# Optimization experiments

Measured on AMD Instinct MI355X. Metric: run time of the kernel, lower is better.

The kernel has to match this reference:

```python
import jax, jax.numpy as jnp
import numpy as np

EPS = 1e-12
LN_EPS = 1e-5
RIDGE = 0.01
M, L, T = 256, 4096, 2048


def setup_inputs() -> dict:
    key = jax.random.key(0)
    ks = jax.random.split(key, 16)
    inp = {
        "gamma": jax.random.uniform(ks[0], (L,), dtype=jnp.float32),
        "A_re": jax.random.normal(ks[1], (M, L), dtype=jnp.float32),
        "A_im": jax.random.normal(ks[2], (M, L), dtype=jnp.float32),
        "X_re": jax.random.normal(ks[3], (M, T), dtype=jnp.float32),
        "X_im": jax.random.normal(ks[4], (M, T), dtype=jnp.float32),
        # LayerNorm(L) params
        "ln_w": jnp.ones((L,), jnp.float32),
        "ln_b": jnp.zeros((L,), jnp.float32),
        # MultiheadAttention(embed_dim=1, num_heads=1): in_proj [3,1]->[3], out_proj [1,1]->[1]
        "in_w": jax.random.normal(ks[5], (3,), dtype=jnp.float32),
        "in_b": jnp.zeros((3,), jnp.float32),
        "out_w": jax.random.normal(ks[6], (1,), dtype=jnp.float32),
        "out_b": jnp.zeros((1,), jnp.float32),
        # gate Linear(L, L)
        "gate_W": jax.random.normal(ks[7], (L, L), dtype=jnp.float32) * (1.0 / np.sqrt(L)),
        "gate_b": jnp.zeros((L,), jnp.float32),
        # learned scalars
        "delta": jnp.float32(0.5),
        "lmbda": jnp.float32(0.01),
    }
    return inp


def _iaa_forward(gamma, A_re, A_im, X_re, X_im, ln_w, ln_b, in_w, in_b,
                 out_w, out_b, gate_W, gate_b, delta, lmbda):
    A = (A_re + 1j * A_im).astype(jnp.complex64)      # [M, L]
    X = (X_re + 1j * X_im).astype(jnp.complex64)      # [M, T]
    p = gamma                                         # [L]

    # R = A diag(p) A^H + ridge * I   (MxM)
    AP = A * p[None, :].astype(A.dtype)
    R = AP @ A.conj().T + RIDGE * jnp.eye(M, dtype=A.dtype)
    Rinv = jnp.linalg.inv(R)                          # [M, M]

    Ah = A.conj().T                                   # [L, M]
    ARi = Ah @ Rinv                                   # [L, M]
    S = ARi @ X                                       # [L, T]
    q = jnp.sum(jnp.abs(S) ** 2, axis=1)              # [L]
    d = jnp.real(jnp.sum(ARi * Ah, axis=1))           # [L]
    v = q / (d + EPS)

    # constrain_gamma -> sigmoid(delta); use_residual
    dlt = jax.nn.sigmoid(delta)
    u = p + dlt * (v - p)

    # LayerNorm over the full length-L vector
    mu = jnp.mean(u)
    var = jnp.mean((u - mu) ** 2)
    u_p = (u - mu) / jnp.sqrt(var + LN_EPS) * ln_w + ln_b

    # MultiheadAttention(embed_dim=1, num_heads=1) over seq of L tokens, scale = 1/sqrt(1) = 1
    qv = u_p * in_w[0] + in_b[0]                      # [L]
    kv = u_p * in_w[1] + in_b[1]
    vv = u_p * in_w[2] + in_b[2]
    scores = qv[:, None] * kv[None, :]                # [L, L]
    attn = jax.nn.softmax(scores, axis=-1)
    attn_out = (attn @ vv) * out_w[0] + out_b[0]      # [L]

    # gating on u (pre-layernorm), as in the torch code
    g = jax.nn.sigmoid(gate_W @ u + gate_b)           # Linear: u @ W.T + b, u is 1-D -> W @ u + b
    r = g * v + (1.0 - g) * p

    s = r + attn_out
    return jax.nn.relu(s - lmbda)


def reference(gamma, A_re, A_im, X_re, X_im, ln_w, ln_b, in_w, in_b,
              out_w, out_b, gate_W, gate_b, delta, lmbda):
    return _iaa_forward(gamma, A_re, A_im, X_re, X_im, ln_w, ln_b, in_w, in_b,
                        out_w, out_b, gate_W, gate_b, delta, lmbda)
```

## Files before the change

### kernel.cpp

```cpp
#include <hip/hip_runtime.h>
#include <hip/hip_bf16.h>
#include <math.h>

#define MM 256
#define LL 4096
#define TT 2048

typedef __attribute__((ext_vector_type(8))) short bf16x8;
typedef __attribute__((ext_vector_type(4))) float f32x4;
typedef __attribute__((ext_vector_type(4))) unsigned short us4;
typedef unsigned short ushort_t;

#define OFF_Q      262144
#define OFF_D      266240
#define OFF_V      270336
#define OFF_U      274432
#define OFF_UP     278528
#define OFF_RINVP  290816
#define OFF_GP     421888
#define OFF_APL    552960
#define OFF_XPL    2650112
#define OFF_ATP    3698688
#define OFF_WTP    5795840
#define OFF_PA     5795840
#define OFF_PX     8417280
#define OFF_E0P    9990144
#define OFF_EAP    10252288
#define OFF_EBP    10514432
#define OFF_XAT    10776576
#define OFF_XBT    10907648

#define MFMA3(ACC, AH, AL, BH, BL)                                              \
  ACC = __builtin_amdgcn_mfma_f32_16x16x32_bf16(AH, BH, ACC, 0, 0, 0);          \
  ACC = __builtin_amdgcn_mfma_f32_16x16x32_bf16(AH, BL, ACC, 0, 0, 0);          \
  ACC = __builtin_amdgcn_mfma_f32_16x16x32_bf16(AL, BH, ACC, 0, 0, 0);

__device__ __forceinline__ void split_bf16(float x, ushort_t& h, ushort_t& l) {
  __hip_bfloat16 bh = __float2bfloat16(x);
  h = *(ushort_t*)&bh;
  __hip_bfloat16 bl = __float2bfloat16(x - __bfloat162float(bh));
  l = *(ushort_t*)&bl;
}
__device__ __forceinline__ float bfu2f(ushort_t u) {
  unsigned v = ((unsigned)u) << 16;
  float f;
  __builtin_memcpy(&f, &v, 4);
  return f;
}

__device__ __forceinline__ void tile_ij(int t, int& ti, int& tj) {
  float f = sqrtf(8.0f * (float)t + 1.0f);
  ti = (int)((f - 1.0f) * 0.5f + 0.001f);
  tj = t - ((ti * (ti + 1)) >> 1);
}

__device__ __forceinline__ float wave_red_sum(float v) {
#pragma unroll
  for (int o = 32; o > 0; o >>= 1) v += __shfl_down(v, o);
  return v;
}
__device__ __forceinline__ float wave_red_max(float v) {
#pragma unroll
  for (int o = 32; o > 0; o >>= 1) v = fmaxf(v, __shfl_down(v, o));
  return v;
}
__device__ float blk_red_sum(float v) {
  __shared__ float sh[4];
  int lane = threadIdx.x & 63, wv = threadIdx.x >> 6;
  v = wave_red_sum(v);
  __syncthreads();
  if (lane == 0) sh[wv] = v;
  __syncthreads();
  return sh[0] + sh[1] + sh[2] + sh[3];
}
__device__ float blk_red_max(float v) {
  __shared__ float shm[4];
  int lane = threadIdx.x & 63, wv = threadIdx.x >> 6;
  v = wave_red_max(v);
  __syncthreads();
  if (lane == 0) shm[wv] = v;
  __syncthreads();
  return fmaxf(fmaxf(shm[0], shm[1]), fmaxf(shm[2], shm[3]));
}

__device__ __forceinline__ float2 r_mirror(const float2* __restrict__ R, int i, int j) {
  if ((i >> 6) >= (j >> 6)) return R[i * 256 + j];
  float2 r = R[j * 256 + i];
  r.y = -r.y;
  return r;
}

__global__ __launch_bounds__(256) void k_prep(float* __restrict__ ws,
                                              const float* __restrict__ Are,
                                              const float* __restrict__ Aim,
                                              const float* __restrict__ Xre,
                                              const float* __restrict__ Xim,
                                              const float* __restrict__ gamma) {
  __shared__ float tr[32][33], ti[32][33];
  int bid = blockIdx.x, tid = threadIdx.x;
  if (bid < 8) {
    ((float4*)(ws + OFF_Q))[bid * 256 + tid] = make_float4(0.f, 0.f, 0.f, 0.f);
  } else if (bid < 1032) {
    int i4 = (bid - 8) * 256 + tid;
    ushort_t* dst = (ushort_t*)(ws + OFF_APL);
    float4 re = ((const float4*)Are)[i4];
    float4 im = ((const float4*)Aim)[i4];
    float4 ga = ((const float4*)gamma)[i4 & (LL / 4 - 1)];
    float sr[4] = {re.x * sqrtf(ga.x), re.y * sqrtf(ga.y), re.z * sqrtf(ga.z), re.w * sqrtf(ga.w)};
    float si[4] = {im.x * sqrtf(ga.x), im.y * sqrtf(ga.y), im.z * sqrtf(ga.z), im.w * sqrtf(ga.w)};
    us4 hr, lr, hi, li;
#pragma unroll
    for (int e = 0; e < 4; ++e) {
      ushort_t h, l;
      split_bf16(sr[e], h, l); hr[e] = h; lr[e] = l;
      split_bf16(si[e], h, l); hi[e] = h; li[e] = l;
    }
    size_t o = (size_t)i4 * 4;
    *(us4*)(dst + o) = hr;
    *(us4*)(dst + (size_t)MM * LL + o) = lr;
    *(us4*)(dst + 2 * (size_t)MM * LL + o) = hi;
    *(us4*)(dst + 3 * (size_t)MM * LL + o) = li;
  } else if (bid < 1544) {
    int i4 = (bid - 1032) * 256 + tid;
    ushort_t* dst = (ushort_t*)(ws + OFF_XPL);
    float4 re = ((const float4*)Xre)[i4];
    float4 im = ((const float4*)Xim)[i4];
    float fr[4] = {re.x, re.y, re.z, re.w};
    float fi[4] = {im.x, im.y, im.z, im.w};
    us4 hr, lr, hi, li;
#pragma unroll
    for (int e = 0; e < 4; ++e) {
      ushort_t h, l;
      split_bf16(fr[e], h, l); hr[e] = h; lr[e] = l;
      split_bf16(fi[e], h, l); hi[e] = h; li[e] = l;
    }
    size_t o = (size_t)i4 * 4;
    *(us4*)(dst + o) = hr;
    *(us4*)(dst + (size_t)MM * TT + o) = lr;
    *(us4*)(dst + 2 * (size_t)MM * TT + o) = hi;
    *(us4*)(dst + 3 * (size_t)MM * TT + o) = li;
  } else {
    int b2 = bid - 1544;
    ushort_t* dst = (ushort_t*)(ws + OFF_ATP);
    int c0 = (b2 & 127) * 32, r0 = (b2 >> 7) * 32;
    int tx = tid & 31, tg = tid >> 5;
#pragma unroll
    for (int i = 0; i < 4; ++i) {
      int r = tg + 8 * i;
      tr[r][tx] = Are[(size_t)(r0 + r) * LL + c0 + tx];
      ti[r][tx] = Aim[(size_t)(r0 + r) * LL + c0 + tx];
    }
    __syncthreads();
#pragma unroll
    for (int i = 0; i < 4; ++i) {
      int rr = tg + 8 * i;
      size_t o = (size_t)(c0 + rr) * 256 + r0 + tx;
      ushort_t h, l;
      split_bf16(tr[tx][rr], h, l);
      dst[o] = h;
      dst[o + 1048576] = l;
      split_bf16(ti[tx][rr], h, l);
      dst[o + 2097152] = h;
      dst[o + 3145728] = l;
    }
  }
}

__global__ __launch_bounds__(256, 4) void k_gram_both(float* __restrict__ ws) {
  __shared__ __align__(16) ushort_t sA[4][64][40];
  __shared__ __align__(16) ushort_t sB[4][64][40];
  const int ti_lu[10] = {0, 1, 1, 2, 2, 2, 3, 3, 3, 3};
  const int tj_lu[10] = {0, 0, 1, 0, 1, 2, 0, 1, 2, 3};
  int bid = blockIdx.x;
  const ushort_t* pl;
  float2* P;
  int K, tile, ksplit;
  size_t PS;
  if (bid < 320) {
    pl = (const ushort_t*)(ws + OFF_APL);
    P = (float2*)(ws + OFF_PA) + (size_t)bid * 4096;
    K = LL;
    PS = (size_t)MM * LL;
    tile = bid % 10;
    ksplit = bid / 10;
  } else {
    int b2 = bid - 320;
    pl = (const ushort_t*)(ws + OFF_XPL);
    P = (float2*)(ws + OFF_PX) + (size_t)b2 * 4096;
    K = TT;
    PS = (size_t)MM * TT;
    tile = b2 % 10;
    ksplit = b2 / 10;
  }
  int kbeg = ksplit * 128;
  int i0 = ti_lu[tile] * 64, j0 = tj_lu[tile] * 64;
  bool diag = (i0 == j0);
  int tid = threadIdx.x;
  int lane = tid & 63, wv = tid >> 6;
  int srow = tid >> 2, sslot = tid & 3;
  int arow = wv * 16 + (lane & 15);
  int kq = (lane >> 4) * 8;
  f32x4 z = {0.f, 0.f, 0.f, 0.f};
  f32x4 Zrr[4], Zri[4], Zir[4], Zii[4];
#pragma unroll
  for (int s = 0; s < 4; ++s) { Zrr[s] = z; Zri[s] = z; Zir[s] = z; Zii[s] = z; }

  for (int chunk = 0; chunk < 4; ++chunk) {
    int k0 = kbeg + chunk * 32;
    __syncthreads();
#pragma unroll
    for (int p = 0; p < 4; ++p) {
      *(bf16x8*)&sA[p][srow][sslot * 8] =
          *(const bf16x8*)(pl + p * PS + (size_t)(i0 + srow) * K + k0 + sslot * 8);
      if (!diag)
        *(bf16x8*)&sB[p][srow][sslot * 8] =
            *(const bf16x8*)(pl + p * PS + (size_t)(j0 + srow) * K + k0 + sslot * 8);
    }
    __syncthreads();
    bf16x8 arh = *(const bf16x8*)&sA[0][arow][kq];
    bf16x8 arl = *(const bf16x8*)&sA[1][arow][kq];
    bf16x8 aih = *(const bf16x8*)&sA[2][arow][kq];
    bf16x8 ail = *(const bf16x8*)&sA[3][arow][kq];
    ushort_t(*bs)[64][40] = diag ? sA : sB;
#pragma unroll
    for (int s = 0; s < 4; ++s) {
      int brow = s * 16 + (lane & 15);
      bf16x8 brh = *(const bf16x8*)&bs[0][brow][kq];
      bf16x8 brl = *(const bf16x8*)&bs[1][brow][kq];
      bf16x8 bih = *(const bf16x8*)&bs[2][brow][kq];
      bf16x8 bil = *(const bf16x8*)&bs[3][brow][kq];
      MFMA3(Zrr[s], arh, arl, brh, brl);
      MFMA3(Zri[s], arh, arl, bih, bil);
      MFMA3(Zir[s], aih, ail, brh, brl);
      MFMA3(Zii[s], aih, ail, bih, bil);
    }
  }
  int lrb = wv * 16 + (lane >> 4) * 4;
#pragma unroll
  for (int s = 0; s < 4; ++s) {
    int lc = s * 16 + (lane & 15);
#pragma unroll
    for (int r = 0; r < 4; ++r) {
      float re = Zrr[s][r] + Zii[s][r];
      float im = Zir[s][r] - Zri[s][r];
      P[(lrb + r) * 64 + lc] = make_float2(re, im);
    }
  }
}

__global__ __launch_bounds__(256) void k_reduce(float* __restrict__ ws) {
  int bid = blockIdx.x, tid = threadIdx.x;
  if (bid < 160) {
    const float2* PA = (const float2*)(ws + OFF_PA);
    float2* R2 = (float2*)ws;
    int t = bid >> 4;
    int e = ((bid & 15) << 8) + tid;
    float sx = 0.f, sy = 0.f;
#pragma unroll 4
    for (int k = 0; k < 32; ++k) {
      float2 p = PA[(size_t)(k * 10 + t) * 4096 + e];
      sx += p.x; sy += p.y;
    }
    int ti, tj;
    tile_ij(t, ti, tj);
    int i = ti * 64 + (e >> 6), j = tj * 64 + (e & 63);
    if (i == j) sx += 0.01f;
    R2[i * 256 + j] = make_float2(sx, sy);
  } else {
    const float2* PX = (const float2*)(ws + OFF_PX);
    ushort_t* dst = (ushort_t*)(ws + OFF_GP);
    int idx = (bid - 160) * 256 + tid;
    int i = idx >> 8, j = idx & 255;
    int ii = i, jj = j;
    float sgn = 1.f;
    if ((i >> 6) < (j >> 6)) { ii = j; jj = i; sgn = -1.f; }
    int ti = ii >> 6, tj = jj >> 6;
    int t = ((ti * (ti + 1)) >> 1) + tj;
    int e = ((ii & 63) << 6) + (jj & 63);
    float sx = 0.f, sy = 0.f;
#pragma unroll 4
    for (int k = 0; k < 16; ++k) {
      float2 p = PX[(size_t)(k * 10 + t) * 4096 + e];
      sx += p.x; sy += p.y;
    }
    sy *= sgn;
    ushort_t h, l;
    split_bf16(sx, h, l);
    dst[idx] = h;
    dst[idx + 65536] = l;
    split_bf16(sy, h, l);
    dst[idx + 131072] = h;
    dst[idx + 196608] = l;
  }
}

__global__ __launch_bounds__(256) void k_n1p(float* __restrict__ ws) {
  const float2* R = (const float2*)ws;
  ushort_t* e0 = (ushort_t*)(ws + OFF_E0P);
  ushort_t* e0t = e0 + 262144;
  ushort_t* x1t = (ushort_t*)(ws + OFF_XAT);
  int idx = blockIdx.x * 256 + threadIdx.x;
  int i = idx >> 8, j = idx & 255;
  float Dii = R[i * 257].x, Djj = R[j * 257].x;
  float2 r = r_mirror(R, i, j);
  float dl = (i == j) ? 1.0f : 0.0f;
  float ex = dl - r.x / Dii, ey = -r.y / Dii;
  float xx = (dl + ex) / Djj, xy = ey / Djj;
  int rm = i * 256 + j, trn = j * 256 + i;
  ushort_t h, l;
  split_bf16(ex, h, l);
  e0[rm] = h; e0[rm + 65536] = l;
  e0t[trn] = h; e0t[trn + 65536] = l;
  split_bf16(ey, h, l);
  e0[rm + 131072] = h; e0[rm + 196608] = l;
  e0t[trn + 131072] = h; e0t[trn + 196608] = l;
  split_bf16(xx, h, l);
  x1t[trn] = h; x1t[trn + 65536] = l;
  split_bf16(xy, h, l);
  x1t[trn + 131072] = h; x1t[trn + 196608] = l;
}

__global__ __launch_bounds__(256) void k_prim(const ushort_t* __restrict__ Arm,
                                              const ushort_t* __restrict__ BtrE,
                                              const ushort_t* __restrict__ BtrX,
                                              const ushort_t* __restrict__ AddX,
                                              ushort_t* __restrict__ EoutRm,
                                              ushort_t* __restrict__ EoutTr,
                                              ushort_t* __restrict__ XoutTr,
                                              ushort_t* __restrict__ XoutRm,
                                              int nEjobs) {
  __shared__ __align__(16) ushort_t sB[4][32][40];
  int job = blockIdx.x;
  bool isE = job < nEjobs;
  int b = isE ? job : job - nEjobs;
  const ushort_t* Bp = isE ? BtrE : BtrX;
  const ushort_t* Add = isE ? (const ushort_t*)nullptr : AddX;
  ushort_t* Otr = isE ? EoutTr : XoutTr;
  ushort_t* Orm = isE ? EoutRm : XoutRm;
  int j0 = (b & 7) * 32, i0 = (b >> 3) * 64;
  int tid = threadIdx.x;
  int lane = tid & 63, wv = tid >> 6;
  int spos = tid & 127;
  int srow = spos >> 2, sslot = spos & 3;
  int p0 = (tid >> 7) * 2;
  int m = i0 + wv * 16 + (lane & 15);
  int kq = (lane >> 4) * 8;
  f32x4 z = {0.f, 0.f, 0.f, 0.f};
  f32x4 Zrr[2], Zri[2], Zir[2], Zii[2];
#pragma unroll
  for (int s = 0; s < 2; ++s) { Zrr[s] = z; Zri[s] = z; Zir[s] = z; Zii[s] = z; }
  for (int k0 = 0; k0 < 256; k0 += 32) {
    __syncthreads();
    {
      size_t bo = (size_t)(j0 + srow) * 256 + k0 + sslot * 8;
      *(bf16x8*)&sB[p0][srow][sslot * 8] =
          *(const bf16x8*)(Bp + (size_t)p0 * 65536 + bo);
      *(bf16x8*)&sB[p0 + 1][srow][sslot * 8] =
          *(const bf16x8*)(Bp + (size_t)(p0 + 1) * 65536 + bo);
    }
    __syncthreads();
    size_t ao = (size_t)m * 256 + k0 + kq;
    bf16x8 arh = *(const bf16x8*)(Arm + ao);
    bf16x8 arl = *(const bf16x8*)(Arm + 65536 + ao);
    bf16x8 aih = *(const bf16x8*)(Arm + 131072 + ao);
    bf16x8 ail = *(const bf16x8*)(Arm + 196608 + ao);
#pragma unroll
    for (int s = 0; s < 2; ++s) {
      int brow = s * 16 + (lane & 15);
      bf16x8 brh = *(const bf16x8*)&sB[0][brow][kq];
      bf16x8 brl = *(const bf16x8*)&sB[1][brow][kq];
      bf16x8 bih = *(const bf16x8*)&sB[2][brow][kq];
      bf16x8 bil = *(const bf16x8*)&sB[3][brow][kq];
      MFMA3(Zrr[s], arh, arl, brh, brl);
      MFMA3(Zri[s], arh, arl, bih, bil);
      MFMA3(Zir[s], aih, ail, brh, brl);
      MFMA3(Zii[s], aih, ail, bih, bil);
    }
  }
  int rbase = i0 + wv * 16 + (lane >> 4) * 4;
#pragma unroll
  for (int s = 0; s < 2; ++s) {
    int col = j0 + s * 16 + (lane & 15);
    size_t wo = (size_t)col * 256 + rbase;
    us4 adr, adl, adi, adj;
    if (Add) {
      adr = *(const us4*)(Add + wo);
      adl = *(const us4*)(Add + 65536 + wo);
      adi = *(const us4*)(Add + 131072 + wo);
      adj = *(const us4*)(Add + 196608 + wo);
    }
    us4 hr, lr, hi, li;
#pragma unroll
    for (int r = 0; r < 4; ++r) {
      float re = Zrr[s][r] - Zii[s][r];
      float im = Zri[s][r] + Zir[s][r];
      if (Add) {
        re += bfu2f(adr[r]) + bfu2f(adl[r]);
        im += bfu2f(adi[r]) + bfu2f(adj[r]);
      }
      ushort_t h, l;
      split_bf16(re, h, l); hr[r] = h; lr[r] = l;
      split_bf16(im, h, l); hi[r] = h; li[r] = l;
    }
    if (Otr) {
      *(us4*)(Otr + wo) = hr;
      *(us4*)(Otr + 65536 + wo) = lr;
      *(us4*)(Otr + 131072 + wo) = hi;
      *(us4*)(Otr + 196608 + wo) = li;
    }
    if (Orm) {
#pragma unroll
      for (int r = 0; r < 4; ++r) {
        size_t o = (size_t)(rbase + r) * 256 + col;
        Orm[o] = hr[r];
        Orm[o + 65536] = lr[r];
        Orm[o + 131072] = hi[r];
        Orm[o + 196608] = li[r];
      }
    }
  }
}

__global__ __launch_bounds__(256) void k_wide_mfma(const ushort_t* __restrict__ Ap,
                                                   const ushort_t* __restrict__ Bp,
                                                   const float* __restrict__ AuxRe,
                                                   const float* __restrict__ AuxIm,
                                                   ushort_t* __restrict__ WTout,
                                                   float* __restrict__ dq, int mode) {
  __shared__ __align__(16) ushort_t sB[4][32][40];
  const ushort_t* arh_p = Ap;
  const ushort_t* arl_p = Ap + 65536;
  const ushort_t* aih_p = Ap + 131072;
  const ushort_t* ail_p = Ap + 196608;
  const ushort_t* brh_p = Bp;
  const ushort_t* brl_p = Bp + 1048576;
  const ushort_t* bih_p = Bp + 2097152;
  const ushort_t* bil_p = Bp + 3145728;
  int job = blockIdx.x;
  int j0 = (job & 127) * 32;
  int i0 = (job >> 7) * 64;
  int tid = threadIdx.x;
  int lane = tid & 63, wv = tid >> 6;
  int spos = tid & 127;
  int srow = spos >> 2, sslot = spos & 3;
  int p0 = (tid >> 7) * 2;
  const ushort_t* bp0 = (p0 == 0) ? brh_p : bih_p;
  const ushort_t* bp1 = (p0 == 0) ? brl_p : bil_p;
  int m = i0 + wv * 16 + (lane & 15);
  int kq = (lane >> 4) * 8;
  f32x4 z = {0.f, 0.f, 0.f, 0.f};
  f32x4 Zrr[2], Zri[2], Zir[2], Zii[2];
#pragma unroll
  for (int s = 0; s < 2; ++s) { Zrr[s] = z; Zri[s] = z; Zir[s] = z; Zii[s] = z; }
  for (int k0 = 0; k0 < 256; k0 += 32) {
    __syncthreads();
    {
      size_t bo = (size_t)(j0 + srow) * 256 + k0 + sslot * 8;
      *(bf16x8*)&sB[p0][srow][sslot * 8] = *(const bf16x8*)(bp0 + bo);
      *(bf16x8*)&sB[p0 + 1][srow][sslot * 8] = *(const bf16x8*)(bp1 + bo);
    }
    __syncthreads();
    size_t ao = (size_t)m * 256 + k0 + kq;
    bf16x8 arh = *(const bf16x8*)(arh_p + ao);
    bf16x8 arl = *(const bf16x8*)(arl_p + ao);
    bf16x8 aih = *(const bf16x8*)(aih_p + ao);
    bf16x8 ail = *(const bf16x8*)(ail_p + ao);
#pragma unroll
    for (int s = 0; s < 2; ++s) {
      int brow = s * 16 + (lane & 15);
      bf16x8 brh = *(const bf16x8*)&sB[0][brow][kq];
      bf16x8 brl = *(const bf16x8*)&sB[1][brow][kq];
      bf16x8 bih = *(const bf16x8*)&sB[2][brow][kq];
      bf16x8 bil = *(const bf16x8*)&sB[3][brow][kq];
      MFMA3(Zrr[s], arh, arl, brh, brl);
      MFMA3(Zri[s], arh, arl, bih, bil);
      MFMA3(Zir[s], aih, ail, brh, brl);
      MFMA3(Zii[s], aih, ail, bih, bil);
    }
  }
  int rbase = i0 + wv * 16 + (lane >> 4) * 4;
#pragma unroll
  for (int s = 0; s < 2; ++s) {
    int col = j0 + s * 16 + (lane & 15);
    size_t wo = (size_t)col * 256 + rbase;
    float part = 0.f;
    if (mode == 0) {
      us4 hr, lr, hi, li;
#pragma unroll
      for (int r = 0; r < 4; ++r) {
        float re = Zrr[s][r] - Zii[s][r];
        float im = Zri[s][r] + Zir[s][r];
        ushort_t h, l;
        split_bf16(re, h, l);
        hr[r] = h; lr[r] = l;
        split_bf16(im, h, l);
        hi[r] = h; li[r] = l;
        size_t o = (size_t)(rbase + r) * LL + col;
        part += re * AuxRe[o] - im * AuxIm[o];
      }
      *(us4*)(WTout + wo) = hr;
      *(us4*)(WTout + 1048576 + wo) = lr;
      *(us4*)(WTout + 2097152 + wo) = hi;
      *(us4*)(WTout + 3145728 + wo) = li;
    } else {
      us4 wh = *(const us4*)(brh_p + wo);
      us4 wl = *(const us4*)(brl_p + wo);
      us4 wih = *(const us4*)(bih_p + wo);
      us4 wil = *(const us4*)(bil_p + wo);
#pragma unroll
      for (int r = 0; r < 4; ++r) {
        float re = Zrr[s][r] - Zii[s][r];
        float im = Zri[s][r] + Zir[s][r];
        float wx = bfu2f(wh[r]) + bfu2f(wl[r]);
        float wy = bfu2f(wih[r]) + bfu2f(wil[r]);
        part += wx * re + wy * im;
      }
    }
    part += __shfl_down(part, 32);
    part += __shfl_down(part, 16);
    if ((lane >> 4) == 0) atomicAdd(dq + col, part);
  }
}

__global__ __launch_bounds__(1024) void k_uvln(float* __restrict__ ws,
                                               const float* __restrict__ gamma,
                                               const float* __restrict__ delta,
                                               const float* __restrict__ lnw,
                                               const float* __restrict__ lnb) {
  __shared__ float sh[16];
  int tid = threadIdx.x, lane = tid & 63, wv = tid >> 6;
  float4 q4 = ((const float4*)(ws + OFF_Q))[tid];
  float4 d4 = ((const float4*)(ws + OFF_D))[tid];
  float4 g4 = ((const float4*)gamma)[tid];
  float dlt = 1.0f / (1.0f + expf(-delta[0]));
  float v0 = q4.x / (d4.x + 1e-12f), v1 = q4.y / (d4.y + 1e-12f);
  float v2 = q4.z / (d4.z + 1e-12f), v3 = q4.w / (d4.w + 1e-12f);
  float u0 = g4.x + dlt * (v0 - g4.x), u1 = g4.y + dlt * (v1 - g4.y);
  float u2 = g4.z + dlt * (v2 - g4.z), u3 = g4.w + dlt * (v3 - g4.w);
  ((float4*)(ws + OFF_V))[tid] = make_float4(v0, v1, v2, v3);
  ((float4*)(ws + OFF_U))[tid] = make_float4(u0, u1, u2, u3);
  float s = wave_red_sum(u0 + u1 + u2 + u3);
  if (lane == 0) sh[wv] = s;
  __syncthreads();
  float mu = 0.f;
#pragma unroll
  for (int w = 0; w < 16; ++w) mu += sh[w];
  mu *= (1.0f / LL);
  __syncthreads();
  float d0 = u0 - mu, d1 = u1 - mu, d2 = u2 - mu, d3 = u3 - mu;
  float s2 = wave_red_sum(d0 * d0 + d1 * d1 + d2 * d2 + d3 * d3);
  if (lane == 0) sh[wv] = s2;
  __syncthreads();
  float var = 0.f;
#pragma unroll
  for (int w = 0; w < 16; ++w) var += sh[w];
  var *= (1.0f / LL);
  float inv = rsqrtf(var + 1e-5f);
  float4 w4 = ((const float4*)lnw)[tid];
  float4 b4 = ((const float4*)lnb)[tid];
  ((float4*)(ws + OFF_UP))[tid] =
      make_float4(d0 * inv * w4.x + b4.x, d1 * inv * w4.y + b4.y,
                  d2 * inv * w4.z + b4.z, d3 * inv * w4.w + b4.w);
}

__global__ __launch_bounds__(256) void k_gateattn(const float* __restrict__ ws,
                                                  const float* __restrict__ Wg,
                                                  const float* __restrict__ gb,
                                                  const float* __restrict__ inw,
                                                  const float* __restrict__ inb,
                                                  const float* __restrict__ outw,
                                                  const float* __restrict__ outb,
                                                  const float* __restrict__ gamma,
                                                  const float* __restrict__ lmbda,
                                                  float* __restrict__ out) {
  const float* uvec = ws + OFF_U;
  const float* up = ws + OFF_UP;
  const float* vvec = ws + OFF_V;
  int i = blockIdx.x, tid = threadIdx.x;
  const float4* wr = (const float4*)(Wg + (size_t)i * LL);
  const float4* u4 = (const float4*)uvec;
  float s = 0.f;
  for (int j = tid; j < LL / 4; j += 256) {
    float4 w = wr[j], x = u4[j];
    s += w.x * x.x + w.y * x.y + w.z * x.z + w.w * x.w;
  }
  float tot = blk_red_sum(s);
  float g = 1.0f / (1.0f + expf(-(tot + gb[i])));
  float qv = up[i] * inw[0] + inb[0];
  float w1 = inw[1], b1 = inb[1], w2 = inw[2], b2 = inb[2];
  const float4* up4 = (const float4*)up;
  float mx = -3.4e38f;
  for (int j = tid; j < LL / 4; j += 256) {
    float4 u = up4[j];
    mx = fmaxf(mx, fmaxf(fmaxf(qv * (u.x * w1 + b1), qv * (u.y * w1 + b1)),
                         fmaxf(qv * (u.z * w1 + b1), qv * (u.w * w1 + b1))));
  }
  mx = blk_red_max(mx);
  float den = 0.f, num = 0.f;
  for (int j = tid; j < LL / 4; j += 256) {
    float4 u = up4[j];
    float e0 = expf(qv * (u.x * w1 + b1) - mx);
    float e1 = expf(qv * (u.y * w1 + b1) - mx);
    float e2 = expf(qv * (u.z * w1 + b1) - mx);
    float e3 = expf(qv * (u.w * w1 + b1) - mx);
    den += e0 + e1 + e2 + e3;
    num += e0 * (u.x * w2 + b2) + e1 * (u.y * w2 + b2) + e2 * (u.z * w2 + b2) + e3 * (u.w * w2 + b2);
  }
  den = blk_red_sum(den);
  num = blk_red_sum(num);
  if (tid == 0) {
    float attn = (num / den) * outw[0] + outb[0];
    float r = g * vvec[i] + (1.0f - g) * gamma[i] + attn - lmbda[0];
    out[i] = fmaxf(r, 0.0f);
  }
}

extern "C" void kernel_launch(void* const* d_in, const int* in_sizes, int n_in,
                              void* d_out, int out_size, void* d_ws, size_t ws_size,
                              hipStream_t stream) {
  const float* gamma = (const float*)d_in[0];
  const float* Are   = (const float*)d_in[1];
  const float* Aim   = (const float*)d_in[2];
  const float* Xre   = (const float*)d_in[3];
  const float* Xim   = (const float*)d_in[4];
  const float* lnw   = (const float*)d_in[5];
  const float* lnb   = (const float*)d_in[6];
  const float* inw   = (const float*)d_in[7];
  const float* inb   = (const float*)d_in[8];
  const float* outw  = (const float*)d_in[9];
  const float* outb  = (const float*)d_in[10];
  const float* gateW = (const float*)d_in[11];
  const float* gateb = (const float*)d_in[12];
  const float* delta = (const float*)d_in[13];
  const float* lmbda = (const float*)d_in[14];
  float* out = (float*)d_out;
  float* ws = (float*)d_ws;

  ushort_t* e0rm = (ushort_t*)(ws + OFF_E0P);
  ushort_t* e0tr = e0rm + 262144;
  ushort_t* eArm = (ushort_t*)(ws + OFF_EAP);
  ushort_t* eAtr = eArm + 262144;
  ushort_t* eBrm = (ushort_t*)(ws + OFF_EBP);
  ushort_t* eBtr = eBrm + 262144;
  ushort_t* xAt = (ushort_t*)(ws + OFF_XAT);
  ushort_t* xBt = (ushort_t*)(ws + OFF_XBT);
  ushort_t* Rinvp = (ushort_t*)(ws + OFF_RINVP);

  k_prep<<<2568, 256, 0, stream>>>(ws, Are, Aim, Xre, Xim, gamma);
  k_gram_both<<<480, 256, 0, stream>>>(ws);
  k_reduce<<<416, 256, 0, stream>>>(ws);
  k_n1p<<<256, 256, 0, stream>>>(ws);
  k_prim<<<32, 256, 0, stream>>>(e0rm, e0tr, nullptr, nullptr,
                                 eArm, eAtr, nullptr, nullptr, 32);
  k_prim<<<64, 256, 0, stream>>>(eArm, eAtr, xAt, xAt,
                                 eBrm, eBtr, xBt, nullptr, 32);
  k_prim<<<64, 256, 0, stream>>>(eBrm, eBtr, xBt, xBt,
                                 eArm, eAtr, xAt, nullptr, 32);
  k_prim<<<64, 256, 0, stream>>>(eArm, eAtr, xAt, xAt,
                                 eBrm, eBtr, xBt, nullptr, 32);
  k_prim<<<32, 256, 0, stream>>>(eBrm, nullptr, xBt, xBt,
                                 nullptr, nullptr, nullptr, Rinvp, 0);
  k_wide_mfma<<<512, 256, 0, stream>>>(Rinvp, (const ushort_t*)(ws + OFF_ATP),
                                       Are, Aim, (ushort_t*)(ws + OFF_WTP),
                                       ws + OFF_D, 0);
  k_wide_mfma<<<512, 256, 0, stream>>>((const ushort_t*)(ws + OFF_GP),
                                       (const ushort_t*)(ws + OFF_WTP),
                                       nullptr, nullptr, nullptr, ws + OFF_Q, 1);
  k_uvln<<<1, 1024, 0, stream>>>(ws, gamma, delta, lnw, lnb);
  k_gateattn<<<LL, 256, 0, stream>>>(ws, gateW, gateb, inw, inb, outw, outb,
                                     gamma, lmbda, out);
}
```

Measured before the change: 256.7 us.

## Fork X-path prep and gram onto second stream; halve k_prim tile width

Splits the prep kernel into an A path and an X path, and moves the X preparation, A transpose, X gram and X reduce onto a second non-blocking stream. Events join it back before the wide MFMA kernels, so the X gram branch can overlap the A gram and the Newton-iteration chain. Separately, k_prim tiles shrink from 32 to 16 columns, doubling the block count on the serial inverse-iteration kernels to fill more CUs, at the cost of more redundant A-operand loads. The side stream adds launch and event overhead and relies on stream ordering for workspace hazards such as the zeroed Q buffer.

```diff
diff --git a/kernel.cpp b/kernel.cpp
--- a/kernel.cpp
+++ b/kernel.cpp
@@ -90,38 +90,42 @@
   return r;
 }
 
-__global__ __launch_bounds__(256) void k_prep(float* __restrict__ ws,
-                                              const float* __restrict__ Are,
-                                              const float* __restrict__ Aim,
-                                              const float* __restrict__ Xre,
-                                              const float* __restrict__ Xim,
-                                              const float* __restrict__ gamma) {
+__global__ __launch_bounds__(256) void k_prep_a(float* __restrict__ ws,
+                                                const float* __restrict__ Are,
+                                                const float* __restrict__ Aim,
+                                                const float* __restrict__ gamma) {
+  int i4 = blockIdx.x * 256 + threadIdx.x;
+  ushort_t* dst = (ushort_t*)(ws + OFF_APL);
+  float4 re = ((const float4*)Are)[i4];
+  float4 im = ((const float4*)Aim)[i4];
+  float4 ga = ((const float4*)gamma)[i4 & (LL / 4 - 1)];
+  float sr[4] = {re.x * sqrtf(ga.x), re.y * sqrtf(ga.y), re.z * sqrtf(ga.z), re.w * sqrtf(ga.w)};
+  float si[4] = {im.x * sqrtf(ga.x), im.y * sqrtf(ga.y), im.z * sqrtf(ga.z), im.w * sqrtf(ga.w)};
+  us4 hr, lr, hi, li;
+#pragma unroll
+  for (int e = 0; e < 4; ++e) {
+    ushort_t h, l;
+    split_bf16(sr[e], h, l); hr[e] = h; lr[e] = l;
+    split_bf16(si[e], h, l); hi[e] = h; li[e] = l;
+  }
+  size_t o = (size_t)i4 * 4;
+  *(us4*)(dst + o) = hr;
+  *(us4*)(dst + (size_t)MM * LL + o) = lr;
+  *(us4*)(dst + 2 * (size_t)MM * LL + o) = hi;
+  *(us4*)(dst + 3 * (size_t)MM * LL + o) = li;
+}
+
+__global__ __launch_bounds__(256) void k_prep_x(float* __restrict__ ws,
+                                                const float* __restrict__ Xre,
+                                                const float* __restrict__ Xim,
+                                                const float* __restrict__ Are,
+                                                const float* __restrict__ Aim) {
   __shared__ float tr[32][33], ti[32][33];
   int bid = blockIdx.x, tid = threadIdx.x;
   if (bid < 8) {
     ((float4*)(ws + OFF_Q))[bid * 256 + tid] = make_float4(0.f, 0.f, 0.f, 0.f);
-  } else if (bid < 1032) {
+  } else if (bid < 520) {
     int i4 = (bid - 8) * 256 + tid;
-    ushort_t* dst = (ushort_t*)(ws + OFF_APL);
-    float4 re = ((const float4*)Are)[i4];
-    float4 im = ((const float4*)Aim)[i4];
-    float4 ga = ((const float4*)gamma)[i4 & (LL / 4 - 1)];
-    float sr[4] = {re.x * sqrtf(ga.x), re.y * sqrtf(ga.y), re.z * sqrtf(ga.z), re.w * sqrtf(ga.w)};
-    float si[4] = {im.x * sqrtf(ga.x), im.y * sqrtf(ga.y), im.z * sqrtf(ga.z), im.w * sqrtf(ga.w)};
-    us4 hr, lr, hi, li;
-#pragma unroll
-    for (int e = 0; e < 4; ++e) {
-      ushort_t h, l;
-      split_bf16(sr[e], h, l); hr[e] = h; lr[e] = l;
-      split_bf16(si[e], h, l); hi[e] = h; li[e] = l;
-    }
-    size_t o = (size_t)i4 * 4;
-    *(us4*)(dst + o) = hr;
-    *(us4*)(dst + (size_t)MM * LL + o) = lr;
-    *(us4*)(dst + 2 * (size_t)MM * LL + o) = hi;
-    *(us4*)(dst + 3 * (size_t)MM * LL + o) = li;
-  } else if (bid < 1544) {
-    int i4 = (bid - 1032) * 256 + tid;
     ushort_t* dst = (ushort_t*)(ws + OFF_XPL);
     float4 re = ((const float4*)Xre)[i4];
     float4 im = ((const float4*)Xim)[i4];
@@ -140,7 +144,7 @@
     *(us4*)(dst + 2 * (size_t)MM * TT + o) = hi;
     *(us4*)(dst + 3 * (size_t)MM * TT + o) = li;
   } else {
-    int b2 = bid - 1544;
+    int b2 = bid - 520;
     ushort_t* dst = (ushort_t*)(ws + OFF_ATP);
     int c0 = (b2 & 127) * 32, r0 = (b2 >> 7) * 32;
     int tx = tid & 31, tg = tid >> 5;
@@ -166,12 +170,12 @@
   }
 }
 
-__global__ __launch_bounds__(256, 4) void k_gram_both(float* __restrict__ ws) {
+__global__ __launch_bounds__(256, 4) void k_gram(float* __restrict__ ws, int b0) {
   __shared__ __align__(16) ushort_t sA[4][64][40];
   __shared__ __align__(16) ushort_t sB[4][64][40];
   const int ti_lu[10] = {0, 1, 1, 2, 2, 2, 3, 3, 3, 3};
   const int tj_lu[10] = {0, 0, 1, 0, 1, 2, 0, 1, 2, 3};
-  int bid = blockIdx.x;
+  int bid = blockIdx.x + b0;
   const ushort_t* pl;
   float2* P;
   int K, tile, ksplit;
@@ -248,8 +252,8 @@
   }
 }
 
-__global__ __launch_bounds__(256) void k_reduce(float* __restrict__ ws) {
-  int bid = blockIdx.x, tid = threadIdx.x;
+__global__ __launch_bounds__(256) void k_reduce(float* __restrict__ ws, int b0) {
+  int bid = blockIdx.x + b0, tid = threadIdx.x;
   if (bid < 160) {
     const float2* PA = (const float2*)(ws + OFF_PA);
     float2* R2 = (float2*)ws;
@@ -329,7 +333,7 @@
                                               ushort_t* __restrict__ XoutTr,
                                               ushort_t* __restrict__ XoutRm,
                                               int nEjobs) {
-  __shared__ __align__(16) ushort_t sB[4][32][40];
+  __shared__ __align__(16) ushort_t sB[4][16][40];
   int job = blockIdx.x;
   bool isE = job < nEjobs;
   int b = isE ? job : job - nEjobs;
@@ -337,86 +341,71 @@
   const ushort_t* Add = isE ? (const ushort_t*)nullptr : AddX;
   ushort_t* Otr = isE ? EoutTr : XoutTr;
   ushort_t* Orm = isE ? EoutRm : XoutRm;
-  int j0 = (b & 7) * 32, i0 = (b >> 3) * 64;
+  int j0 = (b & 15) * 16, i0 = (b >> 4) * 64;
   int tid = threadIdx.x;
   int lane = tid & 63, wv = tid >> 6;
-  int spos = tid & 127;
-  int srow = spos >> 2, sslot = spos & 3;
-  int p0 = (tid >> 7) * 2;
+  int sp = tid >> 6;
+  int srow = (tid >> 2) & 15, sslot = tid & 3;
   int m = i0 + wv * 16 + (lane & 15);
   int kq = (lane >> 4) * 8;
-  f32x4 z = {0.f, 0.f, 0.f, 0.f};
-  f32x4 Zrr[2], Zri[2], Zir[2], Zii[2];
-#pragma unroll
-  for (int s = 0; s < 2; ++s) { Zrr[s] = z; Zri[s] = z; Zir[s] = z; Zii[s] = z; }
+  f32x4 Zrr = {0.f, 0.f, 0.f, 0.f}, Zri = Zrr, Zir = Zrr, Zii = Zrr;
   for (int k0 = 0; k0 < 256; k0 += 32) {
     __syncthreads();
-    {
-      size_t bo = (size_t)(j0 + srow) * 256 + k0 + sslot * 8;
-      *(bf16x8*)&sB[p0][srow][sslot * 8] =
-          *(const bf16x8*)(Bp + (size_t)p0 * 65536 + bo);
-      *(bf16x8*)&sB[p0 + 1][srow][sslot * 8] =
-          *(const bf16x8*)(Bp + (size_t)(p0 + 1) * 65536 + bo);
-    }
+    *(bf16x8*)&sB[sp][srow][sslot * 8] =
+        *(const bf16x8*)(Bp + (size_t)sp * 65536 + (size_t)(j0 + srow) * 256 + k0 + sslot * 8);
     __syncthreads();
     size_t ao = (size_t)m * 256 + k0 + kq;
     bf16x8 arh = *(const bf16x8*)(Arm + ao);
     bf16x8 arl = *(const bf16x8*)(Arm + 65536 + ao);
     bf16x8 aih = *(const bf16x8*)(Arm + 131072 + ao);
     bf16x8 ail = *(const bf16x8*)(Arm + 196608 + ao);
-#pragma unroll
-    for (int s = 0; s < 2; ++s) {
-      int brow = s * 16 + (lane & 15);
-      bf16x8 brh = *(const bf16x8*)&sB[0][brow][kq];
-      bf16x8 brl = *(const bf16x8*)&sB[1][brow][kq];
-      bf16x8 bih = *(const bf16x8*)&sB[2][brow][kq];
-      bf16x8 bil = *(const bf16x8*)&sB[3][brow][kq];
-      MFMA3(Zrr[s], arh, arl, brh, brl);
-      MFMA3(Zri[s], arh, arl, bih, bil);
-      MFMA3(Zir[s], aih, ail, brh, brl);
-      MFMA3(Zii[s], aih, ail, bih, bil);
-    }
+    int brow = lane & 15;
+    bf16x8 brh = *(const bf16x8*)&sB[0][brow][kq];
+    bf16x8 brl = *(const bf16x8*)&sB[1][brow][kq];
+    bf16x8 bih = *(const bf16x8*)&sB[2][brow][kq];
+    bf16x8 bil = *(const bf16x8*)&sB[3][brow][kq];
+    MFMA3(Zrr, arh, arl, brh, brl);
+    MFMA3(Zri, arh, arl, bih, bil);
+    MFMA3(Zir, aih, ail, brh, brl);
+    MFMA3(Zii, aih, ail, bih, bil);
   }
   int rbase = i0 + wv * 16 + (lane >> 4) * 4;
-#pragma unroll
-  for (int s = 0; s < 2; ++s) {
-    int col = j0 + s * 16 + (lane & 15);
-    size_t wo = (size_t)col * 256 + rbase;
-    us4 adr, adl, adi, adj;
+  int col = j0 + (lane & 15);
+  size_t wo = (size_t)col * 256 + rbase;
+  us4 adr, adl, adi, adj;
+  if (Add) {
+    adr = *(const us4*)(Add + wo);
+    adl = *(const us4*)(Add + 65536 + wo);
+    adi = *(const us4*)(Add + 131072 + wo);
+    adj = *(const us4*)(Add + 196608 + wo);
+  }
+  us4 hr, lr, hi, li;
+#pragma unroll
+  for (int r = 0; r < 4; ++r) {
+    float re = Zrr[r] - Zii[r];
+    float im = Zri[r] + Zir[r];
     if (Add) {
-      adr = *(const us4*)(Add + wo);
-      adl = *(const us4*)(Add + 65536 + wo);
-      adi = *(const us4*)(Add + 131072 + wo);
-      adj = *(const us4*)(Add + 196608 + wo);
-    }
-    us4 hr, lr, hi, li;
+      re += bfu2f(adr[r]) + bfu2f(adl[r]);
+      im += bfu2f(adi[r]) + bfu2f(adj[r]);
+    }
+    ushort_t h, l;
+    split_bf16(re, h, l); hr[r] = h; lr[r] = l;
+    split_bf16(im, h, l); hi[r] = h; li[r] = l;
+  }
+  if (Otr) {
+    *(us4*)(Otr + wo) = hr;
+    *(us4*)(Otr + 65536 + wo) = lr;
+    *(us4*)(Otr + 131072 + wo) = hi;
+    *(us4*)(Otr + 196608 + wo) = li;
+  }
+  if (Orm) {
 #pragma unroll
     for (int r = 0; r < 4; ++r) {
-      float re = Zrr[s][r] - Zii[s][r];
-      float im = Zri[s][r] + Zir[s][r];
-      if (Add) {
-        re += bfu2f(adr[r]) + bfu2f(adl[r]);
-        im += bfu2f(adi[r]) + bfu2f(adj[r]);
-      }
-      ushort_t h, l;
-      split_bf16(re, h, l); hr[r] = h; lr[r] = l;
-      split_bf16(im, h, l); hi[r] = h; li[r] = l;
-    }
-    if (Otr) {
-      *(us4*)(Otr + wo) = hr;
-      *(us4*)(Otr + 65536 + wo) = lr;
-      *(us4*)(Otr + 131072 + wo) = hi;
-      *(us4*)(Otr + 196608 + wo) = li;
-    }
-    if (Orm) {
-#pragma unroll
-      for (int r = 0; r < 4; ++r) {
-        size_t o = (size_t)(rbase + r) * 256 + col;
-        Orm[o] = hr[r];
-        Orm[o + 65536] = lr[r];
-        Orm[o + 131072] = hi[r];
-        Orm[o + 196608] = li[r];
-      }
+      size_t o = (size_t)(rbase + r) * 256 + col;
+      Orm[o] = hr[r];
+      Orm[o + 65536] = lr[r];
+      Orm[o + 131072] = hi[r];
+      Orm[o + 196608] = li[r];
     }
   }
 }
@@ -646,23 +635,44 @@
   ushort_t* xBt = (ushort_t*)(ws + OFF_XBT);
   ushort_t* Rinvp = (ushort_t*)(ws + OFF_RINVP);
 
-  k_prep<<<2568, 256, 0, stream>>>(ws, Are, Aim, Xre, Xim, gamma);
-  k_gram_both<<<480, 256, 0, stream>>>(ws);
-  k_reduce<<<416, 256, 0, stream>>>(ws);
+  static hipStream_t s2 = nullptr;
+  static hipEvent_t evFork = nullptr, evA = nullptr, evG = nullptr;
+  if (s2 == nullptr) {
+    (void)hipStreamCreateWithFlags(&s2, hipStreamNonBlocking);
+    (void)hipEventCreateWithFlags(&evFork, hipEventDisableTiming);
+    (void)hipEventCreateWithFlags(&evA, hipEventDisableTiming);
+    (void)hipEventCreateWithFlags(&evG, hipEventDisableTiming);
+  }
+
+  (void)hipEventRecord(evFork, stream);
+  (void)hipStreamWaitEvent(s2, evFork, 0);
+
+  k_prep_x<<<1544, 256, 0, s2>>>(ws, Xre, Xim, Are, Aim);
+  (void)hipEventRecord(evA, s2);
+  k_gram<<<160, 256, 0, s2>>>(ws, 320);
+  k_reduce<<<256, 256, 0, s2>>>(ws, 160);
+  (void)hipEventRecord(evG, s2);
+
+  k_prep_a<<<1024, 256, 0, stream>>>(ws, Are, Aim, gamma);
+  k_gram<<<320, 256, 0, stream>>>(ws, 0);
+  k_reduce<<<160, 256, 0, stream>>>(ws, 0);
   k_n1p<<<256, 256, 0, stream>>>(ws);
-  k_prim<<<32, 256, 0, stream>>>(e0rm, e0tr, nullptr, nullptr,
-                                 eArm, eAtr, nullptr, nullptr, 32);
-  k_prim<<<64, 256, 0, stream>>>(eArm, eAtr, xAt, xAt,
-                                 eBrm, eBtr, xBt, nullptr, 32);
-  k_prim<<<64, 256, 0, stream>>>(eBrm, eBtr, xBt, xBt,
-                                 eArm, eAtr, xAt, nullptr, 32);
-  k_prim<<<64, 256, 0, stream>>>(eArm, eAtr, xAt, xAt,
-                                 eBrm, eBtr, xBt, nullptr, 32);
-  k_prim<<<32, 256, 0, stream>>>(eBrm, nullptr, xBt, xBt,
+  k_prim<<<64, 256, 0, stream>>>(e0rm, e0tr, nullptr, nullptr,
+                                 eArm, eAtr, nullptr, nullptr, 64);
+  k_prim<<<128, 256, 0, stream>>>(eArm, eAtr, xAt, xAt,
+                                  eBrm, eBtr, xBt, nullptr, 64);
+  k_prim<<<128, 256, 0, stream>>>(eBrm, eBtr, xBt, xBt,
+                                  eArm, eAtr, xAt, nullptr, 64);
+  k_prim<<<128, 256, 0, stream>>>(eArm, eAtr, xAt, xAt,
+                                  eBrm, eBtr, xBt, nullptr, 64);
+  k_prim<<<64, 256, 0, stream>>>(eBrm, nullptr, xBt, xBt,
                                  nullptr, nullptr, nullptr, Rinvp, 0);
+
+  (void)hipStreamWaitEvent(stream, evA, 0);
   k_wide_mfma<<<512, 256, 0, stream>>>(Rinvp, (const ushort_t*)(ws + OFF_ATP),
                                        Are, Aim, (ushort_t*)(ws + OFF_WTP),
                                        ws + OFF_D, 0);
+  (void)hipStreamWaitEvent(stream, evG, 0);
   k_wide_mfma<<<512, 256, 0, stream>>>((const ushort_t*)(ws + OFF_GP),
                                        (const ushort_t*)(ws + OFF_WTP),
                                        nullptr, nullptr, nullptr, ws + OFF_Q, 1);
```

Result: slower. 313.9 us (+22.3%).
